# Kernel optimization log

Hardware: AMD Instinct MI355X
Metric: run time of the kernel (lower is better)

The kernel has to match this reference:

```python
import jax, jax.numpy as jnp
import numpy as np

N_NODES = 50000
N_EDGES = 800000
D = 128          # node_state_dim
H = 256          # edge hidden / message dim (= 2*D)
NH = 256         # node MLP hidden


def setup_inputs() -> dict:
    key = jax.random.key(0)
    ks = jax.random.split(key, 20)
    s = 0.05
    inp = {
        "node_states": jax.random.normal(ks[0], (N_NODES, D), jnp.float32),
        "edge_features": jax.random.normal(ks[1], (N_EDGES, 1), jnp.float32),
        "from_idx": jax.random.randint(ks[2], (N_EDGES,), 0, N_NODES, jnp.int32),
        "to_idx": jax.random.randint(ks[3], (N_EDGES,), 0, N_NODES, jnp.int32),
        # forward-direction message net: Linear(2D+1 -> H), ReLU, Linear(H -> H)
        "W1": jax.random.normal(ks[4], (2 * D + 1, H), jnp.float32) * s,
        "b1": jnp.zeros((H,), jnp.float32),
        "W2": jax.random.normal(ks[5], (H, H), jnp.float32) * s,
        "b2": jnp.zeros((H,), jnp.float32),
        # reverse-direction message net (separate params)
        "RW1": jax.random.normal(ks[6], (2 * D + 1, H), jnp.float32) * s,
        "Rb1": jnp.zeros((H,), jnp.float32),
        "RW2": jax.random.normal(ks[7], (H, H), jnp.float32) * s,
        "Rb2": jnp.zeros((H,), jnp.float32),
        # node update MLP: Linear(3D -> NH), ReLU, Linear(NH -> D)
        "Wn1": jax.random.normal(ks[8], (3 * D, NH), jnp.float32) * s,
        "bn1": jnp.zeros((NH,), jnp.float32),
        "Wn2": jax.random.normal(ks[9], (NH, D), jnp.float32) * s,
        "bn2": jnp.zeros((D,), jnp.float32),
    }
    return inp


def _mlp2(x, W1, b1, W2, b2):
    return jax.nn.relu(x @ W1 + b1) @ W2 + b2


def reference(node_states, edge_features, from_idx, to_idx,
              W1, b1, W2, b2, RW1, Rb1, RW2, Rb2, Wn1, bn1, Wn2, bn2):
    n_nodes = node_states.shape[0]
    from_states = node_states[from_idx]            # [E, D]
    to_states = node_states[to_idx]                # [E, D]

    # forward direction: messages go to to_idx
    edge_in = jnp.concatenate([from_states, to_states, edge_features], axis=-1)  # [E, 2D+1]
    msgs = _mlp2(edge_in, W1, b1, W2, b2)                                        # [E, H]
    agg = jax.ops.segment_sum(msgs, to_idx, num_segments=n_nodes)                # [N, H]

    # reverse direction: swap roles, aggregate onto from_idx
    redge_in = jnp.concatenate([to_states, from_states, edge_features], axis=-1)
    rmsgs = _mlp2(redge_in, RW1, Rb1, RW2, Rb2)
    agg = agg + jax.ops.segment_sum(rmsgs, from_idx, num_segments=n_nodes)

    # residual node update: MLP on [agg, node_states] -> [N, D]
    upd_in = jnp.concatenate([agg, node_states], axis=-1)                        # [N, 3D]
    return node_states + _mlp2(upd_in, Wn1, bn1, Wn2, bn2)
```

## Files before the change

### kernel.cpp

```cpp
#include <hip/hip_runtime.h>
#include <hip/hip_bf16.h>


typedef __bf16 bf16;
typedef __attribute__((ext_vector_type(8))) __bf16 bf16x8;
typedef __attribute__((ext_vector_type(4))) __bf16 bf16x4v;
typedef __attribute__((ext_vector_type(4))) float floatx4;
typedef __attribute__((ext_vector_type(2))) float floatx2;

#define DD 128
#define HH 256
#define CAPB 800
#define MAXBINS 3200

__device__ __forceinline__ bf16x8 ns8(const float* __restrict__ NS, int row, int col, int N) {
    bf16x8 v;
    if (row < N) {
        float4 f0 = *(const float4*)&NS[(size_t)row * DD + col];
        float4 f1 = *(const float4*)&NS[(size_t)row * DD + col + 4];
        v[0] = (bf16)f0.x; v[1] = (bf16)f0.y; v[2] = (bf16)f0.z; v[3] = (bf16)f0.w;
        v[4] = (bf16)f1.x; v[5] = (bf16)f1.y; v[6] = (bf16)f1.z; v[7] = (bf16)f1.w;
    } else {
        v = (bf16x8)(bf16)0.0f;
    }
    return v;
}

__global__ void k_pre(const float* __restrict__ W1, const float* __restrict__ RW1,
                      bf16* __restrict__ Wt1, int* __restrict__ gcur, int NBINS) {
    const int b = blockIdx.x, t = threadIdx.x;
    if (b < 512) {
        int idx = b * 256 + t;
        int n = idx >> 7, k = idx & 127;
        float v;
        if (n < 256)      v = W1[k * 256 + n];
        else if (n < 512) v = W1[(128 + k) * 256 + (n - 256)];
        else if (n < 768) v = RW1[k * 256 + (n - 512)];
        else              v = RW1[(128 + k) * 256 + (n - 768)];
        Wt1[idx] = (bf16)v;
    } else {
        int i = (b - 512) * 256 + t;
        if (i < NBINS) gcur[i] = 0;
    }
}

__global__ __launch_bounds__(256) void k_front(
    const float* __restrict__ NS, const int* __restrict__ from_idx,
    const int* __restrict__ to_idx, const float* __restrict__ ef,
    const float* __restrict__ W2, const float* __restrict__ RW2,
    const float* __restrict__ Wn1, const float* __restrict__ Wn2,
    const float* __restrict__ b2, const float* __restrict__ Rb2,
    const bf16* __restrict__ Wt1,
    int* __restrict__ gcur, int2* __restrict__ binbuf,
    unsigned char* __restrict__ Pn, bf16* __restrict__ Pf,
    bf16* __restrict__ Wth, bf16* __restrict__ Wt2,
    float* __restrict__ u, float* __restrict__ ru,
    int E, int N, int NP, int NBINS, int BINB, int MB) {
    __shared__ __align__(16) unsigned char smem[30720];
    const int b = blockIdx.x, t = threadIdx.x;

    if (b < BINB) {
        int* hist = (int*)smem;
        int* base = hist + MAXBINS;
        const int NBF = NP >> 5;
        for (int i = t; i < NBINS; i += 256) hist[i] = 0;
        __syncthreads();
        const int e0 = b * 2048;
        int f[8], tt[8]; float w[8]; bool valid[8];
#pragma unroll
        for (int q = 0; q < 8; ++q) {
            int e = e0 + q * 256 + t;
            valid[q] = e < E;
            int ec = valid[q] ? e : 0;
            f[q] = from_idx[ec]; tt[q] = to_idx[ec]; w[q] = ef[ec];
        }
#pragma unroll
        for (int q = 0; q < 8; ++q) {
            if (valid[q]) {
                atomicAdd(&hist[tt[q] >> 5], 1);
                atomicAdd(&hist[NBF + (f[q] >> 5)], 1);
            }
        }
        __syncthreads();
        for (int i = t; i < NBINS; i += 256) {
            int h = hist[i];
            base[i] = h ? atomicAdd(&gcur[i], h) : 0;
            hist[i] = 0;
        }
        __syncthreads();
#pragma unroll
        for (int q = 0; q < 8; ++q) {
            if (valid[q]) {
                int wb = __float_as_int(w[q]);
                int b1 = tt[q] >> 5;
                int r1 = base[b1] + atomicAdd(&hist[b1], 1);
                if (r1 < CAPB)
                    binbuf[(size_t)b1 * CAPB + r1] = make_int2(((tt[q] & 31) << 17) | f[q], wb);
                int b2i = NBF + (f[q] >> 5);
                int r2 = base[b2i] + atomicAdd(&hist[b2i], 1);
                if (r2 < CAPB)
                    binbuf[(size_t)b2i * CAPB + r2] = make_int2(((f[q] & 31) << 17) | tt[q], wb);
            }
        }
        return;
    }

    if (b < BINB + 769) {
        int bb = b - BINB;
        if (bb < 640) {
            int k = bb, m = t;
            float v;
            if (k < 512) {
                const float* Wsrc = (k < 256) ? W2 : RW2;
                int i = k & 255;
                float acc = 0.f;
                for (int j = 0; j < 256; ++j) acc += Wsrc[i * 256 + j] * Wn1[j * 256 + m];
                v = acc;
            } else {
                v = Wn1[(256 + k - 512) * 256 + m];
            }
            Wth[m * 640 + k] = (bf16)v;
        } else if (bb < 768) {
            int idx = (bb - 640) * 256 + t;
            int n = idx >> 8, k = idx & 255;
            Wt2[idx] = (bf16)Wn2[k * 128 + n];
        } else {
            int m = t;
            float a = 0.f, c2 = 0.f;
            for (int j = 0; j < 256; ++j) {
                float w = Wn1[j * 256 + m];
                a += b2[j] * w;
                c2 += Rb2[j] * w;
            }
            u[m] = a;
            ru[m] = c2;
        }
        return;
    }

    {
        bf16 (*As)[64][40] = (bf16(*)[64][40])smem;
        bf16 (*Bs)[2][64][40] = (bf16(*)[2][64][40])(smem + 10240);
        const int p = b - (BINB + 769);
        const int row0 = (p >> 3) * 64;
        const int colp = (p & 7) * 128;
        const int wv = t >> 6, lane = t & 63;
        const int l15 = lane & 15, quad = lane >> 4;
        const int srow = t >> 2, kc = (t & 3) * 8;
        floatx4 acc[2][4] = {};
        for (int k0 = 0; k0 < DD; k0 += 64) {
            bf16x8 av0 = ns8(NS, row0 + srow, k0 + kc, N);
            bf16x8 av1 = ns8(NS, row0 + srow, k0 + 32 + kc, N);
            bf16x8 bv00 = *(const bf16x8*)&Wt1[(size_t)(colp + srow) * DD + k0 + kc];
            bf16x8 bv01 = *(const bf16x8*)&Wt1[(size_t)(colp + srow) * DD + k0 + 32 + kc];
            bf16x8 bv10 = *(const bf16x8*)&Wt1[(size_t)(colp + 64 + srow) * DD + k0 + kc];
            bf16x8 bv11 = *(const bf16x8*)&Wt1[(size_t)(colp + 64 + srow) * DD + k0 + 32 + kc];
            __syncthreads();
            *(bf16x8*)&As[0][srow][kc] = av0;
            *(bf16x8*)&As[1][srow][kc] = av1;
            *(bf16x8*)&Bs[0][0][srow][kc] = bv00;
            *(bf16x8*)&Bs[0][1][srow][kc] = bv01;
            *(bf16x8*)&Bs[1][0][srow][kc] = bv10;
            *(bf16x8*)&Bs[1][1][srow][kc] = bv11;
            __syncthreads();
#pragma unroll
            for (int h = 0; h < 2; ++h) {
                bf16x8 afr[4];
#pragma unroll
                for (int r = 0; r < 4; ++r)
                    afr[r] = *(const bf16x8*)&As[h][r * 16 + l15][quad * 8];
#pragma unroll
                for (int cp = 0; cp < 2; ++cp) {
                    bf16x8 bfr = *(const bf16x8*)&Bs[cp][h][wv * 16 + l15][quad * 8];
#pragma unroll
                    for (int r = 0; r < 4; ++r)
                        acc[cp][r] = __builtin_amdgcn_mfma_f32_16x16x32_bf16(afr[r], bfr, acc[cp][r], 0, 0, 0);
                }
            }
        }
#pragma unroll
        for (int cp = 0; cp < 2; ++cp) {
            const int ocol = colp + cp * 64 + wv * 16 + l15;
            const int ch = ocol & 255;
            const int half = (ocol >> 9) & 1;
            const bool isNbr = ((ocol >> 8) & 1) == 0;
#pragma unroll
            for (int r = 0; r < 4; ++r)
#pragma unroll
                for (int i = 0; i < 4; ++i) {
                    int orow = row0 + r * 16 + quad * 4 + i;
                    float v = acc[cp][r][i];
                    if (isNbr) {
                        int pk = __builtin_amdgcn_cvt_pk_fp8_f32(v, v, 0, false);
                        Pn[(size_t)orow * 512 + half * 256 + ch] = (unsigned char)(pk & 0xFF);
                    } else {
                        Pf[(size_t)orow * 512 + half * 256 + ch] = (bf16)v;
                    }
                }
        }
    }
}

__global__ __launch_bounds__(256) void k_aggf(
    const unsigned char* __restrict__ Pn, const bf16* __restrict__ Pf,
    const int2* __restrict__ binbuf, const int* __restrict__ gcnt,
    const float* __restrict__ W1, const float* __restrict__ b1,
    const float* __restrict__ RW1, const float* __restrict__ Rb1,
    bf16* __restrict__ S_to, bf16* __restrict__ S_fr,
    int* __restrict__ deg, int NP) {
    __shared__ int hist[32], kstart[32], cur[32], scanbuf[32];
    __shared__ int2 srec[CAPB];
    const int b = blockIdx.x, t = threadIdx.x;
    const int NBF = NP >> 5;
    const bool rev = b >= NBF;
    const int node0 = (rev ? b - NBF : b) << 5;
    int cnt = gcnt[b]; if (cnt > CAPB) cnt = CAPB;
    const int2* bin = binbuf + (size_t)b * CAPB;
    if (t < 32) hist[t] = 0;
    __syncthreads();
    for (int i = t; i < cnt; i += 256)
        atomicAdd(&hist[((unsigned)bin[i].x) >> 17], 1);
    __syncthreads();
    if (t < 32) scanbuf[t] = hist[t];
    __syncthreads();
    for (int d = 1; d < 32; d <<= 1) {
        int v = (t < 32 && t >= d) ? scanbuf[t - d] : 0;
        __syncthreads();
        if (t < 32) scanbuf[t] += v;
        __syncthreads();
    }
    if (t < 32) { kstart[t] = scanbuf[t] - hist[t]; cur[t] = scanbuf[t] - hist[t]; }
    __syncthreads();
    for (int i = t; i < cnt; i += 256) {
        int2 r = bin[i];
        int rk = atomicAdd(&cur[((unsigned)r.x) >> 17], 1);
        srec[rk] = r;
    }
    __syncthreads();
    const int wv = t >> 6, lane = t & 63, c = lane * 4;
    const int fixoff = rev ? 256 : 0;
    const int nbroff = rev ? 256 : 0;
    const float* bb = rev ? Rb1 : b1;
    const float* wl = (rev ? RW1 : W1) + 65536;
    float4 bv = *(const float4*)&bb[c];
    float4 wv4 = *(const float4*)&wl[c];
    bf16* Sarr = rev ? S_fr : S_to;
    for (int key = wv; key < 32; key += 4) {
        int node = node0 + key;
        bf16x4v pf = *(const bf16x4v*)&Pf[(size_t)node * 512 + fixoff + c];
        float fx0 = (float)pf[0] + bv.x;
        float fx1 = (float)pf[1] + bv.y;
        float fx2 = (float)pf[2] + bv.z;
        float fx3 = (float)pf[3] + bv.w;
        int beg = kstart[key], kc2 = hist[key], end = beg + kc2;
        float a0 = 0.f, a1 = 0.f, a2 = 0.f, a3 = 0.f;
        int j = beg;
        for (; j + 8 <= end; j += 8) {
            int2 rr[8]; int qq[8];
#pragma unroll
            for (int z = 0; z < 8; ++z) rr[z] = srec[j + z];
#pragma unroll
            for (int z = 0; z < 8; ++z)
                qq[z] = *(const int*)&Pn[(size_t)(rr[z].x & 0x1FFFF) * 512 + nbroff + c];
#pragma unroll
            for (int z = 0; z < 8; ++z) {
                float w = __int_as_float(rr[z].y);
                floatx2 lo = __builtin_amdgcn_cvt_pk_f32_fp8(qq[z], false);
                floatx2 hi = __builtin_amdgcn_cvt_pk_f32_fp8(qq[z], true);
                a0 += fmaxf(fx0 + lo.x + w * wv4.x, 0.f);
                a1 += fmaxf(fx1 + lo.y + w * wv4.y, 0.f);
                a2 += fmaxf(fx2 + hi.x + w * wv4.z, 0.f);
                a3 += fmaxf(fx3 + hi.y + w * wv4.w, 0.f);
            }
        }
        for (; j < end; ++j) {
            int2 r = srec[j];
            int qq = *(const int*)&Pn[(size_t)(r.x & 0x1FFFF) * 512 + nbroff + c];
            float w = __int_as_float(r.y);
            floatx2 lo = __builtin_amdgcn_cvt_pk_f32_fp8(qq, false);
            floatx2 hi = __builtin_amdgcn_cvt_pk_f32_fp8(qq, true);
            a0 += fmaxf(fx0 + lo.x + w * wv4.x, 0.f);
            a1 += fmaxf(fx1 + lo.y + w * wv4.y, 0.f);
            a2 += fmaxf(fx2 + hi.x + w * wv4.z, 0.f);
            a3 += fmaxf(fx3 + hi.y + w * wv4.w, 0.f);
        }
        bf16x4v o;
        o[0] = (bf16)a0; o[1] = (bf16)a1; o[2] = (bf16)a2; o[3] = (bf16)a3;
        *(bf16x4v*)&Sarr[(size_t)node * 256 + c] = o;
        if (lane == 0) deg[(rev ? NP : 0) + node] = kc2;
    }
}

__global__ __launch_bounds__(256) void k_node(
    const bf16* __restrict__ S_to, const bf16* __restrict__ S_fr,
    const float* __restrict__ NS, const bf16* __restrict__ Wth,
    const bf16* __restrict__ Wt2,
    const float* __restrict__ u, const float* __restrict__ ru,
    const float* __restrict__ bn1, const float* __restrict__ bn2,
    const int* __restrict__ deg, float* __restrict__ out, int NP, int N) {
    __shared__ __align__(16) unsigned char smem[33792];
    bf16 (*As)[40]  = (bf16(*)[40])smem;
    bf16 (*Bs)[40]  = (bf16(*)[40])(smem + 5120);
    bf16 (*Hs)[264] = (bf16(*)[264])smem;
    const int tid = threadIdx.x;
    const int wv = tid >> 6, lane = tid & 63;
    const int l15 = lane & 15, quad = lane >> 4;
    const int row0 = blockIdx.x * 64;
    const int srow = tid >> 2, kc = (tid & 3) * 8;
    floatx4 acc[4][4] = {};
    const int arow = row0 + srow;
    for (int k0 = 0; k0 < 640; k0 += 32) {
        bf16x8 av;
        if (k0 < 512) {
            const bf16* S = (k0 < 256) ? S_to : S_fr;
            av = *(const bf16x8*)&S[(size_t)arow * 256 + (k0 & 255) + kc];
        } else {
            av = ns8(NS, arow, (k0 - 512) + kc, N);
        }
        bf16x8 bv[4];
#pragma unroll
        for (int j = 0; j < 4; ++j)
            bv[j] = *(const bf16x8*)&Wth[(size_t)(srow + 64 * j) * 640 + k0 + kc];
        __syncthreads();
        *(bf16x8*)&As[srow][kc] = av;
#pragma unroll
        for (int j = 0; j < 4; ++j)
            *(bf16x8*)&Bs[srow + 64 * j][kc] = bv[j];
        __syncthreads();
#pragma unroll
        for (int s = 0; s < 4; ++s) {
            bf16x8 bfr = *(const bf16x8*)&Bs[wv * 64 + s * 16 + l15][quad * 8];
#pragma unroll
            for (int r = 0; r < 4; ++r) {
                bf16x8 afr = *(const bf16x8*)&As[r * 16 + l15][quad * 8];
                acc[s][r] = __builtin_amdgcn_mfma_f32_16x16x32_bf16(afr, bfr, acc[s][r], 0, 0, 0);
            }
        }
    }
    __syncthreads();
#pragma unroll
    for (int s = 0; s < 4; ++s) {
        int col = wv * 64 + s * 16 + l15;
        float uc = u[col], rc = ru[col], bc = bn1[col];
#pragma unroll
        for (int r = 0; r < 4; ++r)
#pragma unroll
            for (int i = 0; i < 4; ++i) {
                int row = r * 16 + quad * 4 + i;
                float v = acc[s][r][i] + (float)deg[row0 + row] * uc
                        + (float)deg[NP + row0 + row] * rc + bc;
                Hs[row][col] = (bf16)fmaxf(v, 0.f);
            }
    }
    __syncthreads();
    floatx4 acc2[2][4] = {};
    for (int k0 = 0; k0 < HH; k0 += 32) {
        bf16x8 afr[4];
#pragma unroll
        for (int r = 0; r < 4; ++r)
            afr[r] = *(const bf16x8*)&Hs[r * 16 + l15][k0 + quad * 8];
#pragma unroll
        for (int s = 0; s < 2; ++s) {
            int col = wv * 32 + s * 16 + l15;
            bf16x8 bfr = *(const bf16x8*)&Wt2[(size_t)col * HH + k0 + quad * 8];
#pragma unroll
            for (int r = 0; r < 4; ++r)
                acc2[s][r] = __builtin_amdgcn_mfma_f32_16x16x32_bf16(afr[r], bfr, acc2[s][r], 0, 0, 0);
        }
    }
#pragma unroll
    for (int s = 0; s < 2; ++s) {
        int ocol = wv * 32 + s * 16 + l15;
        float bb = bn2[ocol];
#pragma unroll
        for (int r = 0; r < 4; ++r)
#pragma unroll
            for (int i = 0; i < 4; ++i) {
                int orow = row0 + r * 16 + quad * 4 + i;
                if (orow < N)
                    out[(size_t)orow * DD + ocol] = acc2[s][r][i] + bb + NS[(size_t)orow * DD + ocol];
            }
    }
}

extern "C" void kernel_launch(void* const* d_in, const int* in_sizes, int n_in,
                              void* d_out, int out_size, void* d_ws, size_t ws_size,
                              hipStream_t stream) {
    const float* NS   = (const float*)d_in[0];
    const float* ef   = (const float*)d_in[1];
    const int* from_idx = (const int*)d_in[2];
    const int* to_idx   = (const int*)d_in[3];
    const float* W1  = (const float*)d_in[4];
    const float* b1  = (const float*)d_in[5];
    const float* W2  = (const float*)d_in[6];
    const float* b2  = (const float*)d_in[7];
    const float* RW1 = (const float*)d_in[8];
    const float* Rb1 = (const float*)d_in[9];
    const float* RW2 = (const float*)d_in[10];
    const float* Rb2 = (const float*)d_in[11];
    const float* Wn1 = (const float*)d_in[12];
    const float* bn1 = (const float*)d_in[13];
    const float* Wn2 = (const float*)d_in[14];
    const float* bn2 = (const float*)d_in[15];

    const int N  = in_sizes[0] / DD;
    const int E  = in_sizes[2];
    const int NP = ((N + 63) / 64) * 64;
    const int MB = NP / 64;
    const int NBF = NP / 32;
    const int NBINS = 2 * NBF;
    const int BINB = (E + 2047) / 2048;
    const int FRONT = BINB + 769 + 8 * MB;
    const int PREB = 512 + (NBINS + 255) / 256;

    char* base = (char*)d_ws;
    size_t off_b = 0;
    auto alloc = [&](size_t b) { size_t o = off_b; off_b += (b + 255) & ~(size_t)255; return o; };
    unsigned char* Pn = (unsigned char*)(base + alloc((size_t)NP * 512));
    bf16* Pf   = (bf16*)(base + alloc((size_t)NP * 512 * 2));
    bf16* S_to = (bf16*)(base + alloc((size_t)NP * 256 * 2));
    bf16* S_fr = (bf16*)(base + alloc((size_t)NP * 256 * 2));
    int* deg   = (int*)(base + alloc((size_t)2 * NP * 4));
    int* gcur  = (int*)(base + alloc((size_t)NBINS * 4));
    int2* binbuf = (int2*)(base + alloc((size_t)NBINS * CAPB * 8));
    bf16* Wt1 = (bf16*)(base + alloc(1024 * 128 * 2));
    bf16* Wth = (bf16*)(base + alloc(256 * 640 * 2));
    bf16* Wt2 = (bf16*)(base + alloc(128 * 256 * 2));
    float* u  = (float*)(base + alloc(256 * 4));
    float* ru = (float*)(base + alloc(256 * 4));

    k_pre<<<PREB, 256, 0, stream>>>(W1, RW1, Wt1, gcur, NBINS);
    k_front<<<FRONT, 256, 0, stream>>>(NS, from_idx, to_idx, ef,
                                       W2, RW2, Wn1, Wn2, b2, Rb2, Wt1,
                                       gcur, binbuf, Pn, Pf, Wth, Wt2, u, ru,
                                       E, N, NP, NBINS, BINB, MB);
    k_aggf<<<NBINS, 256, 0, stream>>>(Pn, Pf, binbuf, gcur, W1, b1, RW1, Rb1,
                                      S_to, S_fr, deg, NP);
    k_node<<<MB, 256, 0, stream>>>(S_to, S_fr, NS, Wth, Wt2, u, ru, bn1, bn2,
                                   deg, (float*)d_out, NP, N);
}
```

Baseline: 321.3 us.

## Split aggf wave into half-waves over edges with packed f32 math

The aggregation kernel now has each half-wave handle a different edge, with each lane covering 8 channels through 8-byte gathers and packed f32 add/fma instructions. The two halves are combined with a cross-lane shuffle before storing. The bin records are loaded once into registers and reused for both the histogram and scatter passes. The node-projection GEMM blocks are also reordered so 8 column tiles of a row group run adjacently, which should improve cache reuse of the A tile. The aim is fewer instructions and better memory-level parallelism in the gather, at the cost of a shuffle reduction and masked tail handling.

```diff
diff --git a/kernel.cpp b/kernel.cpp
--- a/kernel.cpp
+++ b/kernel.cpp
@@ -12,6 +12,17 @@
 #define HH 256
 #define CAPB 800
 #define MAXBINS 3200
+
+__device__ __forceinline__ floatx2 pk_add(floatx2 a, floatx2 b) {
+    floatx2 d;
+    asm("v_pk_add_f32 %0, %1, %2" : "=v"(d) : "v"(a), "v"(b));
+    return d;
+}
+__device__ __forceinline__ floatx2 pk_fma(floatx2 a, floatx2 b, floatx2 c) {
+    floatx2 d;
+    asm("v_pk_fma_f32 %0, %1, %2, %3" : "=v"(d) : "v"(a), "v"(b), "v"(c));
+    return d;
+}
 
 __device__ __forceinline__ bf16x8 ns8(const float* __restrict__ NS, int row, int col, int N) {
     bf16x8 v;
@@ -142,8 +153,10 @@
         bf16 (*As)[64][40] = (bf16(*)[64][40])smem;
         bf16 (*Bs)[2][64][40] = (bf16(*)[2][64][40])(smem + 10240);
         const int p = b - (BINB + 769);
-        const int row0 = (p >> 3) * 64;
-        const int colp = (p & 7) * 128;
+        const int g = (p >> 6) * 8 + (p & 7);
+        if (g >= MB) return;
+        const int row0 = g * 64;
+        const int colp = ((p >> 3) & 7) * 128;
         const int wv = t >> 6, lane = t & 63;
         const int l15 = lane & 15, quad = lane >> 4;
         const int srow = t >> 2, kc = (t & 3) * 8;
@@ -218,8 +231,12 @@
     const int2* bin = binbuf + (size_t)b * CAPB;
     if (t < 32) hist[t] = 0;
     __syncthreads();
-    for (int i = t; i < cnt; i += 256)
-        atomicAdd(&hist[((unsigned)bin[i].x) >> 17], 1);
+    int2 h0 = make_int2(0, 0), h1 = h0, h2 = h0, h3 = h0;
+    const bool p0 = t < cnt, p1 = t + 256 < cnt, p2 = t + 512 < cnt, p3 = t + 768 < cnt;
+    if (p0) { h0 = bin[t];       atomicAdd(&hist[((unsigned)h0.x) >> 17], 1); }
+    if (p1) { h1 = bin[t + 256]; atomicAdd(&hist[((unsigned)h1.x) >> 17], 1); }
+    if (p2) { h2 = bin[t + 512]; atomicAdd(&hist[((unsigned)h2.x) >> 17], 1); }
+    if (p3) { h3 = bin[t + 768]; atomicAdd(&hist[((unsigned)h3.x) >> 17], 1); }
     __syncthreads();
     if (t < 32) scanbuf[t] = hist[t];
     __syncthreads();
@@ -231,62 +248,106 @@
     }
     if (t < 32) { kstart[t] = scanbuf[t] - hist[t]; cur[t] = scanbuf[t] - hist[t]; }
     __syncthreads();
-    for (int i = t; i < cnt; i += 256) {
-        int2 r = bin[i];
-        int rk = atomicAdd(&cur[((unsigned)r.x) >> 17], 1);
-        srec[rk] = r;
-    }
-    __syncthreads();
-    const int wv = t >> 6, lane = t & 63, c = lane * 4;
+    if (p0) srec[atomicAdd(&cur[((unsigned)h0.x) >> 17], 1)] = h0;
+    if (p1) srec[atomicAdd(&cur[((unsigned)h1.x) >> 17], 1)] = h1;
+    if (p2) srec[atomicAdd(&cur[((unsigned)h2.x) >> 17], 1)] = h2;
+    if (p3) srec[atomicAdd(&cur[((unsigned)h3.x) >> 17], 1)] = h3;
+    __syncthreads();
+
+    const int wv = t >> 6, lane = t & 63;
+    const int half = lane >> 5, l32 = lane & 31, c = l32 * 8;
     const int fixoff = rev ? 256 : 0;
     const int nbroff = rev ? 256 : 0;
     const float* bb = rev ? Rb1 : b1;
-    const float* wl = (rev ? RW1 : W1) + 65536;
-    float4 bv = *(const float4*)&bb[c];
-    float4 wv4 = *(const float4*)&wl[c];
+    const float* wlrow = (rev ? RW1 : W1) + 65536;
+    float4 bvA = *(const float4*)&bb[c];
+    float4 bvB = *(const float4*)&bb[c + 4];
+    float4 wA = *(const float4*)&wlrow[c];
+    float4 wB = *(const float4*)&wlrow[c + 4];
+    const floatx2 wl01 = {wA.x, wA.y}, wl23 = {wA.z, wA.w};
+    const floatx2 wl45 = {wB.x, wB.y}, wl67 = {wB.z, wB.w};
     bf16* Sarr = rev ? S_fr : S_to;
+    const unsigned char* Pbase = Pn + nbroff + c;
+
     for (int key = wv; key < 32; key += 4) {
-        int node = node0 + key;
-        bf16x4v pf = *(const bf16x4v*)&Pf[(size_t)node * 512 + fixoff + c];
-        float fx0 = (float)pf[0] + bv.x;
-        float fx1 = (float)pf[1] + bv.y;
-        float fx2 = (float)pf[2] + bv.z;
-        float fx3 = (float)pf[3] + bv.w;
-        int beg = kstart[key], kc2 = hist[key], end = beg + kc2;
-        float a0 = 0.f, a1 = 0.f, a2 = 0.f, a3 = 0.f;
+        const int node = node0 + key;
+        bf16x8 pf = *(const bf16x8*)&Pf[(size_t)node * 512 + fixoff + c];
+        const floatx2 fx01 = {(float)pf[0] + bvA.x, (float)pf[1] + bvA.y};
+        const floatx2 fx23 = {(float)pf[2] + bvA.z, (float)pf[3] + bvA.w};
+        const floatx2 fx45 = {(float)pf[4] + bvB.x, (float)pf[5] + bvB.y};
+        const floatx2 fx67 = {(float)pf[6] + bvB.z, (float)pf[7] + bvB.w};
+        const int beg = kstart[key], kc2 = hist[key], end = beg + kc2;
+        floatx2 a01 = {0.f, 0.f}, a23 = {0.f, 0.f}, a45 = {0.f, 0.f}, a67 = {0.f, 0.f};
         int j = beg;
         for (; j + 8 <= end; j += 8) {
-            int2 rr[8]; int qq[8];
-#pragma unroll
-            for (int z = 0; z < 8; ++z) rr[z] = srec[j + z];
-#pragma unroll
-            for (int z = 0; z < 8; ++z)
-                qq[z] = *(const int*)&Pn[(size_t)(rr[z].x & 0x1FFFF) * 512 + nbroff + c];
-#pragma unroll
-            for (int z = 0; z < 8; ++z) {
-                float w = __int_as_float(rr[z].y);
-                floatx2 lo = __builtin_amdgcn_cvt_pk_f32_fp8(qq[z], false);
-                floatx2 hi = __builtin_amdgcn_cvt_pk_f32_fp8(qq[z], true);
-                a0 += fmaxf(fx0 + lo.x + w * wv4.x, 0.f);
-                a1 += fmaxf(fx1 + lo.y + w * wv4.y, 0.f);
-                a2 += fmaxf(fx2 + hi.x + w * wv4.z, 0.f);
-                a3 += fmaxf(fx3 + hi.y + w * wv4.w, 0.f);
-            }
-        }
-        for (; j < end; ++j) {
-            int2 r = srec[j];
-            int qq = *(const int*)&Pn[(size_t)(r.x & 0x1FFFF) * 512 + nbroff + c];
-            float w = __int_as_float(r.y);
-            floatx2 lo = __builtin_amdgcn_cvt_pk_f32_fp8(qq, false);
-            floatx2 hi = __builtin_amdgcn_cvt_pk_f32_fp8(qq, true);
-            a0 += fmaxf(fx0 + lo.x + w * wv4.x, 0.f);
-            a1 += fmaxf(fx1 + lo.y + w * wv4.y, 0.f);
-            a2 += fmaxf(fx2 + hi.x + w * wv4.z, 0.f);
-            a3 += fmaxf(fx3 + hi.y + w * wv4.w, 0.f);
-        }
-        bf16x4v o;
-        o[0] = (bf16)a0; o[1] = (bf16)a1; o[2] = (bf16)a2; o[3] = (bf16)a3;
-        *(bf16x4v*)&Sarr[(size_t)node * 256 + c] = o;
+            int2 rr[4]; uint2 qv[4];
+#pragma unroll
+            for (int z = 0; z < 4; ++z) rr[z] = srec[j + 2 * z + half];
+#pragma unroll
+            for (int z = 0; z < 4; ++z)
+                qv[z] = *(const uint2*)(Pbase + ((size_t)((((unsigned)rr[z].x) & 0x1FFFFu) << 9)));
+#pragma unroll
+            for (int z = 0; z < 4; ++z) {
+                const float w = __int_as_float(rr[z].y);
+                const floatx2 wp = {w, w};
+                floatx2 n01 = __builtin_amdgcn_cvt_pk_f32_fp8(qv[z].x, false);
+                floatx2 n23 = __builtin_amdgcn_cvt_pk_f32_fp8(qv[z].x, true);
+                floatx2 n45 = __builtin_amdgcn_cvt_pk_f32_fp8(qv[z].y, false);
+                floatx2 n67 = __builtin_amdgcn_cvt_pk_f32_fp8(qv[z].y, true);
+                floatx2 t01 = pk_fma(wp, wl01, pk_add(fx01, n01));
+                floatx2 t23 = pk_fma(wp, wl23, pk_add(fx23, n23));
+                floatx2 t45 = pk_fma(wp, wl45, pk_add(fx45, n45));
+                floatx2 t67 = pk_fma(wp, wl67, pk_add(fx67, n67));
+                floatx2 r01 = {fmaxf(t01.x, 0.f), fmaxf(t01.y, 0.f)};
+                floatx2 r23 = {fmaxf(t23.x, 0.f), fmaxf(t23.y, 0.f)};
+                floatx2 r45 = {fmaxf(t45.x, 0.f), fmaxf(t45.y, 0.f)};
+                floatx2 r67 = {fmaxf(t67.x, 0.f), fmaxf(t67.y, 0.f)};
+                a01 = pk_add(a01, r01);
+                a23 = pk_add(a23, r23);
+                a45 = pk_add(a45, r45);
+                a67 = pk_add(a67, r67);
+            }
+        }
+        for (; j < end; j += 2) {
+            const int ri = j + half;
+            const bool valid = ri < end;
+            int2 r = srec[valid ? ri : beg];
+            const float m = valid ? 1.f : 0.f;
+            const floatx2 mp = {m, m};
+            uint2 q = *(const uint2*)(Pbase + ((size_t)((((unsigned)r.x) & 0x1FFFFu) << 9)));
+            const float w = __int_as_float(r.y);
+            const floatx2 wp = {w, w};
+            floatx2 n01 = __builtin_amdgcn_cvt_pk_f32_fp8(q.x, false);
+            floatx2 n23 = __builtin_amdgcn_cvt_pk_f32_fp8(q.x, true);
+            floatx2 n45 = __builtin_amdgcn_cvt_pk_f32_fp8(q.y, false);
+            floatx2 n67 = __builtin_amdgcn_cvt_pk_f32_fp8(q.y, true);
+            floatx2 t01 = pk_fma(wp, wl01, pk_add(fx01, n01));
+            floatx2 t23 = pk_fma(wp, wl23, pk_add(fx23, n23));
+            floatx2 t45 = pk_fma(wp, wl45, pk_add(fx45, n45));
+            floatx2 t67 = pk_fma(wp, wl67, pk_add(fx67, n67));
+            floatx2 r01 = {fmaxf(t01.x, 0.f), fmaxf(t01.y, 0.f)};
+            floatx2 r23 = {fmaxf(t23.x, 0.f), fmaxf(t23.y, 0.f)};
+            floatx2 r45 = {fmaxf(t45.x, 0.f), fmaxf(t45.y, 0.f)};
+            floatx2 r67 = {fmaxf(t67.x, 0.f), fmaxf(t67.y, 0.f)};
+            a01 = pk_fma(mp, r01, a01);
+            a23 = pk_fma(mp, r23, a23);
+            a45 = pk_fma(mp, r45, a45);
+            a67 = pk_fma(mp, r67, a67);
+        }
+        float s0 = a01.x + __shfl_xor(a01.x, 32);
+        float s1 = a01.y + __shfl_xor(a01.y, 32);
+        float s2 = a23.x + __shfl_xor(a23.x, 32);
+        float s3 = a23.y + __shfl_xor(a23.y, 32);
+        float s4 = a45.x + __shfl_xor(a45.x, 32);
+        float s5 = a45.y + __shfl_xor(a45.y, 32);
+        float s6 = a67.x + __shfl_xor(a67.x, 32);
+        float s7 = a67.y + __shfl_xor(a67.y, 32);
+        if (half == 0) {
+            bf16x8 o;
+            o[0] = (bf16)s0; o[1] = (bf16)s1; o[2] = (bf16)s2; o[3] = (bf16)s3;
+            o[4] = (bf16)s4; o[5] = (bf16)s5; o[6] = (bf16)s6; o[7] = (bf16)s7;
+            *(bf16x8*)&Sarr[(size_t)node * 256 + c] = o;
+        }
         if (lane == 0) deg[(rev ? NP : 0) + node] = kc2;
     }
 }
@@ -410,7 +471,7 @@
     const int NBF = NP / 32;
     const int NBINS = 2 * NBF;
     const int BINB = (E + 2047) / 2048;
-    const int FRONT = BINB + 769 + 8 * MB;
+    const int FRONT = BINB + 769 + 64 * ((MB + 7) / 8);
     const int PREB = 512 + (NBINS + 255) / 256;
 
     char* base = (char*)d_ws;
```

Result: no change. 327.1 us (+1.8%).
